# Kernel optimization log

Measured on AMD Instinct MI355X. Metric: run time of the kernel, lower is better.

The kernel has to match this reference:

```python
import jax, jax.numpy as jnp
import numpy as np

B, T, S = 4, 16, 4096
H, KV, D, DIM = 32, 8, 128, 4096
BASE = 10000.0
START = 2048
SCALE = 1.0 / np.sqrt(D)


def _rope(t, cos, sin):
    # t: [B, T, nh, D]; ggml 'normal' rope rotates adjacent pairs (x[2i], x[2i+1])
    b, tt, nh, d = t.shape
    t2 = t.reshape(b, tt, nh, d // 2, 2)
    x0, x1 = t2[..., 0], t2[..., 1]
    c = cos[None, :, None, :]  # [1, T, 1, D/2]
    s = sin[None, :, None, :]
    r = jnp.stack([x0 * c - x1 * s, x0 * s + x1 * c], axis=-1)
    return r.reshape(b, tt, nh, d)


def setup_inputs() -> dict:
    key = jax.random.key(0)
    ks = jax.random.split(key, 8)
    x = jax.random.normal(ks[0], (B, T, DIM), dtype=jnp.float32)
    k_cache = jax.random.normal(ks[1], (B, S, KV, D), dtype=jnp.float32)
    v_cache = jax.random.normal(ks[2], (B, S, KV, D), dtype=jnp.float32)
    wq = jax.random.normal(ks[3], (H * D, DIM), dtype=jnp.float32) * 0.02
    wk = jax.random.normal(ks[4], (KV * D, DIM), dtype=jnp.float32) * 0.02
    wv = jax.random.normal(ks[5], (KV * D, DIM), dtype=jnp.float32) * 0.02
    wo = jax.random.normal(ks[6], (DIM, H * D), dtype=jnp.float32) * 0.02
    input_pos = jnp.arange(T, dtype=jnp.int32) + START  # contiguous decode chunk
    inv_freq = BASE ** (-jnp.arange(0, D, 2, dtype=jnp.float32) / D)  # [D/2]
    ang = input_pos.astype(jnp.float32)[:, None] * inv_freq[None, :]  # [T, D/2]
    freqs_cos = jnp.cos(ang)
    freqs_sin = jnp.sin(ang)
    # causal mask: kv position <= query absolute position, [T, S] bool
    attn_mask = jnp.arange(S, dtype=jnp.int32)[None, :] <= input_pos[:, None]
    return {"x": x, "freqs_cos": freqs_cos, "freqs_sin": freqs_sin,
            "input_pos": input_pos, "attn_mask": attn_mask,
            "k_cache": k_cache, "v_cache": v_cache,
            "wq": wq, "wk": wk, "wv": wv, "wo": wo}


def reference(x, freqs_cos, freqs_sin, input_pos, attn_mask, k_cache, v_cache, wq, wk, wv, wo):
    b, t, _ = x.shape
    q = (x @ wq.T).reshape(b, t, H, D)
    k = (x @ wk.T).reshape(b, t, KV, D)
    v = (x @ wv.T).reshape(b, t, KV, D)
    q = _rope(q, freqs_cos, freqs_sin)
    k = _rope(k, freqs_cos, freqs_sin)
    # KV-cache scatter (index_copy_ along dim 1)
    kc = k_cache.at[:, input_pos].set(k)  # [B, S, KV, D]
    vc = v_cache.at[:, input_pos].set(v)
    g = H // KV
    qh = q.transpose(0, 2, 1, 3).reshape(b, KV, g, t, D)  # [B, KV, g, T, D]
    kf = kc.transpose(0, 2, 1, 3)  # [B, KV, S, D]
    vf = vc.transpose(0, 2, 1, 3)
    scores = jnp.einsum('bkgtd,bksd->bkgts', qh, kf) * SCALE
    scores = jnp.where(attn_mask[None, None, None], scores, jnp.finfo(scores.dtype).min)
    probs = jax.nn.softmax(scores, axis=-1)
    y = jnp.einsum('bkgts,bksd->bkgtd', probs, vf)  # [B, KV, g, T, D]
    y = y.reshape(b, H, t, D).transpose(0, 2, 1, 3).reshape(b, t, H * D)
    return y @ wo.T
```

## Files before the change

kernel.cpp:

```cpp
#include <hip/hip_runtime.h>
#include <hip/hip_bf16.h>


#define SCALE_F 0.08838834764831845f

typedef __attribute__((ext_vector_type(8))) short bf16x8;
typedef __attribute__((ext_vector_type(4))) float f32x4;

__device__ __forceinline__ unsigned short f2b(float f) {
    __hip_bfloat16 h = __float2bfloat16(f);
    return *reinterpret_cast<unsigned short*>(&h);
}

__device__ __forceinline__ bf16x8 pack8(float4 a, float4 b) {
    bf16x8 r;
    r[0] = (short)f2b(a.x); r[1] = (short)f2b(a.y); r[2] = (short)f2b(a.z); r[3] = (short)f2b(a.w);
    r[4] = (short)f2b(b.x); r[5] = (short)f2b(b.y); r[6] = (short)f2b(b.z); r[7] = (short)f2b(b.w);
    return r;
}

__device__ __forceinline__ void gl_lds16(const void* g, void* l) {
    __builtin_amdgcn_global_load_lds(
        (const __attribute__((address_space(1))) void*)g,
        (__attribute__((address_space(3))) void*)l, 16, 0, 0);
}

__global__ __launch_bounds__(256) void xcvt_kernel(
    const float* __restrict__ x, unsigned short* __restrict__ xb)
{
    const int i = (blockIdx.x * 256 + threadIdx.x) * 4;
    float4 v = *(const float4*)(x + i);
    ushort4 o; o.x = f2b(v.x); o.y = f2b(v.y); o.z = f2b(v.z); o.w = f2b(v.w);
    *(ushort4*)(xb + i) = o;
}

__global__ __launch_bounds__(256) void qkv_gemm_kernel(
    const unsigned short* __restrict__ xb,
    const float* __restrict__ wq, const float* __restrict__ wk, const float* __restrict__ wvp,
    float* __restrict__ part)
{
    __shared__ float wlds[2][16][256];
    const int tid = threadIdx.x, lane = tid & 63, wid = tid >> 6;
    const int l15 = lane & 15, lh = lane >> 4;
    const int n0 = blockIdx.x * 32;
    const int kbase = blockIdx.y * 256;

    const float* wptr; int nn;
    if (n0 < 4096)      { wptr = wq;  nn = n0; }
    else if (n0 < 5120) { wptr = wk;  nn = n0 - 4096; }
    else                { wptr = wvp; nn = n0 - 5120; }

    bf16x8 aq[8];
    {
        const unsigned short* ap = xb + (size_t)(16 * wid + l15) * 4096 + kbase + 8 * lh;
        #pragma unroll
        for (int t = 0; t < 8; ++t) aq[t] = *(const bf16x8*)(ap + t * 32);
    }
    asm volatile("" ::: "memory");

    #pragma unroll
    for (int g = 0; g < 2; ++g) {
        #pragma unroll
        for (int i = 0; i < 4; ++i) {
            const int r = wid * 4 + i;
            const float* src = wptr + (size_t)(nn + g * 16 + r) * 4096 + kbase
                             + ((lane ^ (r & 7)) * 4);
            gl_lds16(src, &wlds[g][r][0]);
        }
        asm volatile("" ::: "memory");
    }

    f32x4 acc[2];
    acc[0] = (f32x4){0.f,0.f,0.f,0.f};
    acc[1] = (f32x4){0.f,0.f,0.f,0.f};

    const int key = l15 & 7;
    #pragma unroll
    for (int g = 0; g < 2; ++g) {
        if (g == 0) asm volatile("s_waitcnt vmcnt(4)" ::: "memory");
        else        asm volatile("s_waitcnt vmcnt(0)" ::: "memory");
        __builtin_amdgcn_s_barrier();
        const float* wrow = &wlds[g][l15][0];
        #pragma unroll
        for (int t = 0; t < 8; ++t) {
            const int c0 = (t * 8 + 2 * lh) ^ key;
            const int c1 = (t * 8 + 2 * lh + 1) ^ key;
            float4 w0 = *(const float4*)(wrow + c0 * 4);
            float4 w1 = *(const float4*)(wrow + c1 * 4);
            bf16x8 b = pack8(w0, w1);
            acc[g] = __builtin_amdgcn_mfma_f32_16x16x32_bf16(aq[t], b, acc[g], 0, 0, 0);
        }
    }

    float* pp = part + (size_t)blockIdx.y * 64 * 6144 + n0;
    #pragma unroll
    for (int g = 0; g < 2; ++g)
        #pragma unroll
        for (int r = 0; r < 4; ++r)
            pp[(16 * wid + 4 * lh + r) * 6144 + g * 16 + l15] = acc[g][r];
}

__global__ __launch_bounds__(256) void qkv_reduce_kernel(
    const float* __restrict__ part,
    const float* __restrict__ fcos, const float* __restrict__ fsin,
    unsigned short* __restrict__ q_out, unsigned short* __restrict__ k_new,
    unsigned short* __restrict__ v_new)
{
    const int gid = blockIdx.x * 256 + threadIdx.x;
    const int m = gid / 1536;
    const int n = (gid % 1536) * 4;
    float4 s = {0.f,0.f,0.f,0.f};
    #pragma unroll
    for (int sp = 0; sp < 16; ++sp) {
        float4 v = *(const float4*)(part + (size_t)(sp * 64 + m) * 6144 + n);
        s.x += v.x; s.y += v.y; s.z += v.z; s.w += v.w;
    }
    const int t = m & 15, b = m >> 4;
    ushort4 o;
    if (n < 5120) {
        int d = n & 127;
        float c0 = fcos[t * 64 + (d >> 1)],     s0 = fsin[t * 64 + (d >> 1)];
        float c1 = fcos[t * 64 + (d >> 1) + 1], s1 = fsin[t * 64 + (d >> 1) + 1];
        o.x = f2b(s.x * c0 - s.y * s0);
        o.y = f2b(s.x * s0 + s.y * c0);
        o.z = f2b(s.z * c1 - s.w * s1);
        o.w = f2b(s.z * s1 + s.w * c1);
    } else {
        o.x = f2b(s.x); o.y = f2b(s.y); o.z = f2b(s.z); o.w = f2b(s.w);
    }
    if (n < 4096) {
        int h = n >> 7, d = n & 127;
        int row = (b * 8 + (h >> 2)) * 64 + (h & 3) * 16 + t;
        *(ushort4*)(q_out + row * 128 + d) = o;
    } else if (n < 5120) {
        int idx = n - 4096, kvh = idx >> 7, d = idx & 127;
        *(ushort4*)(k_new + ((b * 8 + kvh) * 16 + t) * 128 + d) = o;
    } else {
        int idx = n - 5120, kvh = idx >> 7, d = idx & 127;
        *(ushort4*)(v_new + ((b * 8 + kvh) * 16 + t) * 128 + d) = o;
    }
}

__global__ __launch_bounds__(256) void attn_kernel(
    const float* __restrict__ k_cache, const float* __restrict__ v_cache,
    const unsigned short* __restrict__ q_glob,
    const unsigned short* __restrict__ k_new, const unsigned short* __restrict__ v_new,
    float* __restrict__ y_part, float* __restrict__ ml)
{
    __shared__ unsigned short smem[32256];
    unsigned short* kv_lds = smem;
    unsigned short* p_lds  = smem + 21504;

    const int bk = blockIdx.x >> 4;
    const int c  = blockIdx.x & 15;
    const int b = bk >> 3, kvh = bk & 7;
    const int tid = threadIdx.x, lane = tid & 63, wid = tid >> 6;
    const int s0 = c * 128;
    const bool last = (c == 15);

    bf16x8 aq[4];
    {
        const unsigned short* qp = q_glob + (bk * 64 + 16 * wid + (lane & 15)) * 128 + 8 * (lane >> 4);
        #pragma unroll
        for (int kk = 0; kk < 4; ++kk) aq[kk] = *(const bf16x8*)(qp + kk * 32);
    }

    const int rr = tid >> 5, ln4 = (tid & 31) * 4;
    {
        const float* kb = k_cache + ((size_t)(b * 4096 + s0) * 8 + kvh) * 128;
        #pragma unroll 4
        for (int it = 0; it < 16; ++it) {
            int srow = it * 8 + rr;
            float4 kf = *(const float4*)(kb + (size_t)srow * 1024 + ln4);
            ushort4 k4; k4.x = f2b(kf.x); k4.y = f2b(kf.y); k4.z = f2b(kf.z); k4.w = f2b(kf.w);
            *(ushort4*)&kv_lds[srow * 136 + ln4] = k4;
        }
        if (last) {
            int row = tid >> 4, c8 = (tid & 15) * 8;
            *(bf16x8*)&kv_lds[(128 + row) * 136 + c8] =
                *(const bf16x8*)(k_new + (bk * 16 + row) * 128 + c8);
        }
    }
    __syncthreads();

    f32x4 sc[9];
    f32x4 zero4 = {0.f,0.f,0.f,0.f};
    #pragma unroll
    for (int st = 0; st < 9; ++st) sc[st] = zero4;
    #pragma unroll
    for (int kk = 0; kk < 4; ++kk) {
        #pragma unroll
        for (int st = 0; st < 9; ++st) {
            if (st == 8 && !last) continue;
            bf16x8 bf = *(bf16x8*)&kv_lds[(st * 16 + (lane & 15)) * 136 + kk * 32 + 8 * (lane >> 4)];
            sc[st] = __builtin_amdgcn_mfma_f32_16x16x32_bf16(aq[kk], bf, sc[st], 0, 0, 0);
        }
    }

    float mrow[4], lrow[4];
    #pragma unroll
    for (int r = 0; r < 4; ++r) {
        int trow = 4 * (lane >> 4) + r;
        float mx = -3.0e38f;
        #pragma unroll
        for (int st = 0; st < 9; ++st) {
            if (st == 8 && !last) continue;
            float s = sc[st][r] * SCALE_F;
            if (st == 8 && (lane & 15) > trow) s = -3.0e38f;
            sc[st][r] = s;
            mx = fmaxf(mx, s);
        }
        mx = fmaxf(mx, __shfl_xor(mx, 1));
        mx = fmaxf(mx, __shfl_xor(mx, 2));
        mx = fmaxf(mx, __shfl_xor(mx, 4));
        mx = fmaxf(mx, __shfl_xor(mx, 8));
        float sum = 0.f;
        #pragma unroll
        for (int st = 0; st < 9; ++st) {
            if (st == 8 && !last) continue;
            float p = __expf(sc[st][r] - mx);
            sc[st][r] = p;
            sum += p;
        }
        sum += __shfl_xor(sum, 1);
        sum += __shfl_xor(sum, 2);
        sum += __shfl_xor(sum, 4);
        sum += __shfl_xor(sum, 8);
        mrow[r] = mx; lrow[r] = sum;
    }

    #pragma unroll
    for (int st = 0; st < 9; ++st) {
        if (st == 8 && !last) continue;
        #pragma unroll
        for (int r = 0; r < 4; ++r)
            p_lds[(16 * wid + 4 * (lane >> 4) + r) * 168 + st * 16 + (lane & 15)] = f2b(sc[st][r]);
    }
    if ((lane & 15) == 0) {
        #pragma unroll
        for (int r = 0; r < 4; ++r) {
            int row = 16 * wid + 4 * (lane >> 4) + r;
            ml[(bk * 16 + c) * 128 + row * 2 + 0] = mrow[r];
            ml[(bk * 16 + c) * 128 + row * 2 + 1] = lrow[r];
        }
    }
    __syncthreads();

    {
        const float* vb = v_cache + ((size_t)(b * 4096 + s0) * 8 + kvh) * 128;
        #pragma unroll 4
        for (int it = 0; it < 16; ++it) {
            int srow = it * 8 + rr;
            float4 vf = *(const float4*)(vb + (size_t)srow * 1024 + ln4);
            kv_lds[(ln4 + 0) * 168 + srow] = f2b(vf.x);
            kv_lds[(ln4 + 1) * 168 + srow] = f2b(vf.y);
            kv_lds[(ln4 + 2) * 168 + srow] = f2b(vf.z);
            kv_lds[(ln4 + 3) * 168 + srow] = f2b(vf.w);
        }
        if (last) {
            int row = tid >> 4, c8 = (tid & 15) * 8;
            bf16x8 vv = *(const bf16x8*)(v_new + (bk * 16 + row) * 128 + c8);
            #pragma unroll
            for (int u = 0; u < 8; ++u)
                kv_lds[(c8 + u) * 168 + 128 + row] = (unsigned short)vv[u];
            int pr = tid >> 2, pc = (tid & 3) * 4;
            #pragma unroll
            for (int u = 0; u < 4; ++u) p_lds[pr * 168 + 144 + pc + u] = 0;
            int vr = tid >> 1, vc = (tid & 1) * 8;
            #pragma unroll
            for (int u = 0; u < 8; ++u) kv_lds[vr * 168 + 144 + vc + u] = 0;
        }
    }
    __syncthreads();

    f32x4 o_[8];
    #pragma unroll
    for (int nt = 0; nt < 8; ++nt) o_[nt] = zero4;
    #pragma unroll
    for (int ks = 0; ks < 5; ++ks) {
        if (ks == 4 && !last) continue;
        bf16x8 a = *(bf16x8*)&p_lds[(16 * wid + (lane & 15)) * 168 + ks * 32 + 8 * (lane >> 4)];
        #pragma unroll
        for (int nt = 0; nt < 8; ++nt) {
            bf16x8 bf = *(bf16x8*)&kv_lds[(nt * 16 + (lane & 15)) * 168 + ks * 32 + 8 * (lane >> 4)];
            o_[nt] = __builtin_amdgcn_mfma_f32_16x16x32_bf16(a, bf, o_[nt], 0, 0, 0);
        }
    }
    float* yp = y_part + (size_t)(bk * 16 + c) * 8192;
    #pragma unroll
    for (int nt = 0; nt < 8; ++nt) {
        #pragma unroll
        for (int r = 0; r < 4; ++r)
            yp[(16 * wid + 4 * (lane >> 4) + r) * 128 + nt * 16 + (lane & 15)] = o_[nt][r];
    }
}

__global__ __launch_bounds__(256) void combine_kernel(
    const float* __restrict__ y_part, const float* __restrict__ ml,
    unsigned short* __restrict__ y_attn)
{
    const int bid = blockIdx.x;
    const int bk = bid >> 3, rg = bid & 7;
    const int b = bk >> 3, kvh = bk & 7;
    const int tid = threadIdx.x;
    const int d = tid & 127, r2 = tid >> 7;
    for (int rr = 0; rr < 8; rr += 2) {
        int row = rg * 8 + rr + r2;
        float mv[16], lv[16], M = -3.0e38f;
        #pragma unroll
        for (int cc = 0; cc < 16; ++cc) {
            mv[cc] = ml[(bk * 16 + cc) * 128 + row * 2 + 0];
            lv[cc] = ml[(bk * 16 + cc) * 128 + row * 2 + 1];
            M = fmaxf(M, mv[cc]);
        }
        float den = 0.f, acc = 0.f;
        #pragma unroll
        for (int cc = 0; cc < 16; ++cc) {
            float co = __expf(mv[cc] - M);
            den += co * lv[cc];
            acc += co * y_part[((size_t)(bk * 16 + cc) * 64 + row) * 128 + d];
        }
        float y = acc / den;
        int gi = row >> 4, t = row & 15;
        y_attn[(b * 16 + t) * 4096 + (kvh * 4 + gi) * 128 + d] = f2b(y);
    }
}

__global__ __launch_bounds__(256) void proj_gemm_kernel(
    const unsigned short* __restrict__ y_attn, const float* __restrict__ wo,
    float* __restrict__ part)
{
    __shared__ float wlds[2][16][256];
    const int tid = threadIdx.x, lane = tid & 63, wid = tid >> 6;
    const int l15 = lane & 15, lh = lane >> 4;
    const int n0 = blockIdx.x * 32;
    const int kbase = blockIdx.y * 256;

    bf16x8 aq[8];
    {
        const unsigned short* ap = y_attn + (size_t)(16 * wid + l15) * 4096 + kbase + 8 * lh;
        #pragma unroll
        for (int t = 0; t < 8; ++t) aq[t] = *(const bf16x8*)(ap + t * 32);
    }
    asm volatile("" ::: "memory");

    #pragma unroll
    for (int g = 0; g < 2; ++g) {
        #pragma unroll
        for (int i = 0; i < 4; ++i) {
            const int r = wid * 4 + i;
            const float* src = wo + (size_t)(n0 + g * 16 + r) * 4096 + kbase
                             + ((lane ^ (r & 7)) * 4);
            gl_lds16(src, &wlds[g][r][0]);
        }
        asm volatile("" ::: "memory");
    }

    f32x4 acc[2];
    acc[0] = (f32x4){0.f,0.f,0.f,0.f};
    acc[1] = (f32x4){0.f,0.f,0.f,0.f};

    const int key = l15 & 7;
    #pragma unroll
    for (int g = 0; g < 2; ++g) {
        if (g == 0) asm volatile("s_waitcnt vmcnt(4)" ::: "memory");
        else        asm volatile("s_waitcnt vmcnt(0)" ::: "memory");
        __builtin_amdgcn_s_barrier();
        const float* wrow = &wlds[g][l15][0];
        #pragma unroll
        for (int t = 0; t < 8; ++t) {
            const int c0 = (t * 8 + 2 * lh) ^ key;
            const int c1 = (t * 8 + 2 * lh + 1) ^ key;
            float4 w0 = *(const float4*)(wrow + c0 * 4);
            float4 w1 = *(const float4*)(wrow + c1 * 4);
            bf16x8 b = pack8(w0, w1);
            acc[g] = __builtin_amdgcn_mfma_f32_16x16x32_bf16(aq[t], b, acc[g], 0, 0, 0);
        }
    }

    float* pp = part + (size_t)blockIdx.y * 64 * 4096 + n0;
    #pragma unroll
    for (int g = 0; g < 2; ++g)
        #pragma unroll
        for (int r = 0; r < 4; ++r)
            pp[(16 * wid + 4 * lh + r) * 4096 + g * 16 + l15] = acc[g][r];
}

__global__ __launch_bounds__(256) void proj_reduce_kernel(
    const float* __restrict__ part, float* __restrict__ out)
{
    const int gid = blockIdx.x * 256 + threadIdx.x;
    const int m = gid >> 10;
    const int n = (gid & 1023) * 4;
    float4 s = {0.f,0.f,0.f,0.f};
    #pragma unroll
    for (int sp = 0; sp < 16; ++sp) {
        float4 v = *(const float4*)(part + (size_t)(sp * 64 + m) * 4096 + n);
        s.x += v.x; s.y += v.y; s.z += v.z; s.w += v.w;
    }
    *(float4*)(out + (size_t)m * 4096 + n) = s;
}

extern "C" void kernel_launch(void* const* d_in, const int* in_sizes, int n_in,
                              void* d_out, int out_size, void* d_ws, size_t ws_size,
                              hipStream_t stream)
{
    const float* x       = (const float*)d_in[0];
    const float* fcos    = (const float*)d_in[1];
    const float* fsin    = (const float*)d_in[2];
    const float* k_cache = (const float*)d_in[5];
    const float* v_cache = (const float*)d_in[6];
    const float* wq      = (const float*)d_in[7];
    const float* wk      = (const float*)d_in[8];
    const float* wv      = (const float*)d_in[9];
    const float* wo      = (const float*)d_in[10];

    char* p = (char*)d_ws;
    unsigned short* q_out  = (unsigned short*)p; p += 4 * 8 * 64 * 128 * 2;
    unsigned short* k_new  = (unsigned short*)p; p += 4 * 8 * 16 * 128 * 2;
    unsigned short* v_new  = (unsigned short*)p; p += 4 * 8 * 16 * 128 * 2;
    unsigned short* y_attn = (unsigned short*)p; p += 64 * 4096 * 2;
    unsigned short* x_bf16 = (unsigned short*)p; p += 64 * 4096 * 2;
    float* mlbuf  = (float*)p; p += 32 * 16 * 64 * 2 * 4;
    float* y_part = (float*)p; p += (size_t)32 * 16 * 64 * 128 * 4;
    float* bigbuf = (float*)p;

    xcvt_kernel<<<256, 256, 0, stream>>>(x, x_bf16);
    qkv_gemm_kernel<<<dim3(192, 16), 256, 0, stream>>>(x_bf16, wq, wk, wv, bigbuf);
    qkv_reduce_kernel<<<384, 256, 0, stream>>>(bigbuf, fcos, fsin, q_out, k_new, v_new);
    attn_kernel<<<512, 256, 0, stream>>>(k_cache, v_cache, q_out, k_new, v_new, y_part, mlbuf);
    combine_kernel<<<256, 256, 0, stream>>>(y_part, mlbuf, y_attn);
    proj_gemm_kernel<<<dim3(128, 16), 256, 0, stream>>>(y_attn, wo, bigbuf);
    proj_reduce_kernel<<<256, 256, 0, stream>>>(bigbuf, (float*)d_out);
}
```

Before: 97.39 us.

## Pipeline GEMM K-loop with 4-stage LDS ring and swizzled bf16 activation layout

Both skinny GEMMs now walk a 512-wide K slice per block in 32-element chunks. Weight and activation tiles are streamed into a 4-buffer LDS ring with async global-to-LDS loads issued two chunks ahead, replacing the old single-shot 256-wide load. The split-K factor drops from 16 to 8, which halves the partial-sum traffic in the reduce kernels but also halves the grid and the parallelism. Activations (x and y_attn) are written in a chunked, XOR-swizzled layout so each chunk is one contiguous copy into LDS, and the per-chunk barriers add sync overhead.

```diff
diff --git a/kernel.cpp b/kernel.cpp
--- a/kernel.cpp
+++ b/kernel.cpp
@@ -25,79 +25,87 @@
         (__attribute__((address_space(3))) void*)l, 16, 0, 0);
 }
 
+
 __global__ __launch_bounds__(256) void xcvt_kernel(
     const float* __restrict__ x, unsigned short* __restrict__ xb)
 {
-    const int i = (blockIdx.x * 256 + threadIdx.x) * 4;
-    float4 v = *(const float4*)(x + i);
-    ushort4 o; o.x = f2b(v.x); o.y = f2b(v.y); o.z = f2b(v.z); o.w = f2b(v.w);
-    *(ushort4*)(xb + i) = o;
-}
+    const int flat = blockIdx.x * 256 + threadIdx.x;
+    const int m = flat >> 9, rem = flat & 511;
+    const int c = rem >> 2, j = rem & 3;
+    const float* src = x + (size_t)m * 4096 + c * 32 + j * 8;
+    float4 a = *(const float4*)src, b = *(const float4*)(src + 4);
+    *(bf16x8*)(xb + c * 2048 + m * 32 + ((j ^ (m & 3)) * 8)) = pack8(a, b);
+}
+
+#define GEMM_BODY(WPTR, NN, LDW, APTR, CG_BASE, NCHUNK, ACC)                                   \
+    const int l15 = lane & 15, lh = lane >> 4;                                                 \
+    const int wr8 = lane >> 3, wc8 = lane & 7;                                                 \
+    const float* wsrc = (WPTR) + (size_t)((NN) + 8 * wid + wr8) * (LDW)                        \
+                      + ((wc8 ^ (wr8 & 7)) * 4);                                               \
+    const unsigned short* asrc = (APTR) + (size_t)(CG_BASE) * 2048 + wid * 512 + lane * 8;     \
+    float* wdst = &wlds[0][0] + wid * 256;                                \
+    unsigned short* adst = &alds[0][0] + wid * 512;                     \
+    _Pragma("unroll")                                                                          \
+    for (int pc = 0; pc < 2; ++pc) {                                                           \
+        gl_lds16(wsrc + (size_t)pc * 32, wdst + (size_t)pc * 1024);                            \
+        gl_lds16(asrc + (size_t)pc * 2048, adst + (size_t)pc * 2048);                          \
+    }                                                                                          \
+    const int key = l15 & 7;                                                                   \
+    const int akey = (l15 & 3);                                                                \
+    for (int c = 0; c < (NCHUNK); ++c) {                                                       \
+        if (c + 2 < (NCHUNK)) {                                                                \
+            const int bq = (c + 2) & 3;                                                        \
+            gl_lds16(wsrc + (size_t)(c + 2) * 32, wdst + (size_t)bq * 1024);                   \
+            gl_lds16(asrc + (size_t)(c + 2) * 2048, adst + (size_t)bq * 2048);                 \
+        }                                                                                      \
+        if (c + 2 < (NCHUNK))      asm volatile("s_waitcnt vmcnt(4)" ::: "memory");            \
+        else if (c + 1 < (NCHUNK)) asm volatile("s_waitcnt vmcnt(2)" ::: "memory");            \
+        else                       asm volatile("s_waitcnt vmcnt(0)" ::: "memory");            \
+        __builtin_amdgcn_s_barrier();                                                          \
+        const int buf = c & 3;                                                                 \
+        const float* wt = &wlds[buf][0];                                                       \
+        const unsigned short* at = &alds[buf][0];                                              \
+        const int arow = 16 * wid + l15;                                                       \
+        bf16x8 a = *(const bf16x8*)(at + arow * 32 + ((lh ^ akey) * 8));                       \
+        const float* w0p = wt + l15 * 32;                                                      \
+        const float* w1p = wt + (16 + l15) * 32;                                               \
+        const int c0 = ((2 * lh) ^ key) * 4, c1 = ((2 * lh + 1) ^ key) * 4;                    \
+        bf16x8 b0 = pack8(*(const float4*)(w0p + c0), *(const float4*)(w0p + c1));             \
+        bf16x8 b1 = pack8(*(const float4*)(w1p + c0), *(const float4*)(w1p + c1));             \
+        ACC[0] = __builtin_amdgcn_mfma_f32_16x16x32_bf16(a, b0, ACC[0], 0, 0, 0);              \
+        ACC[1] = __builtin_amdgcn_mfma_f32_16x16x32_bf16(a, b1, ACC[1], 0, 0, 0);              \
+        __builtin_amdgcn_s_barrier();                                                          \
+    }
 
 __global__ __launch_bounds__(256) void qkv_gemm_kernel(
     const unsigned short* __restrict__ xb,
     const float* __restrict__ wq, const float* __restrict__ wk, const float* __restrict__ wvp,
     float* __restrict__ part)
 {
-    __shared__ float wlds[2][16][256];
+    __shared__ float wlds[4][1024];
+    __shared__ unsigned short alds[4][2048];
     const int tid = threadIdx.x, lane = tid & 63, wid = tid >> 6;
-    const int l15 = lane & 15, lh = lane >> 4;
     const int n0 = blockIdx.x * 32;
-    const int kbase = blockIdx.y * 256;
+    const int split = blockIdx.y;
 
     const float* wptr; int nn;
     if (n0 < 4096)      { wptr = wq;  nn = n0; }
     else if (n0 < 5120) { wptr = wk;  nn = n0 - 4096; }
     else                { wptr = wvp; nn = n0 - 5120; }
 
-    bf16x8 aq[8];
-    {
-        const unsigned short* ap = xb + (size_t)(16 * wid + l15) * 4096 + kbase + 8 * lh;
-        #pragma unroll
-        for (int t = 0; t < 8; ++t) aq[t] = *(const bf16x8*)(ap + t * 32);
-    }
-    asm volatile("" ::: "memory");
-
-    #pragma unroll
-    for (int g = 0; g < 2; ++g) {
-        #pragma unroll
-        for (int i = 0; i < 4; ++i) {
-            const int r = wid * 4 + i;
-            const float* src = wptr + (size_t)(nn + g * 16 + r) * 4096 + kbase
-                             + ((lane ^ (r & 7)) * 4);
-            gl_lds16(src, &wlds[g][r][0]);
-        }
-        asm volatile("" ::: "memory");
-    }
-
     f32x4 acc[2];
     acc[0] = (f32x4){0.f,0.f,0.f,0.f};
     acc[1] = (f32x4){0.f,0.f,0.f,0.f};
 
-    const int key = l15 & 7;
-    #pragma unroll
-    for (int g = 0; g < 2; ++g) {
-        if (g == 0) asm volatile("s_waitcnt vmcnt(4)" ::: "memory");
-        else        asm volatile("s_waitcnt vmcnt(0)" ::: "memory");
-        __builtin_amdgcn_s_barrier();
-        const float* wrow = &wlds[g][l15][0];
-        #pragma unroll
-        for (int t = 0; t < 8; ++t) {
-            const int c0 = (t * 8 + 2 * lh) ^ key;
-            const int c1 = (t * 8 + 2 * lh + 1) ^ key;
-            float4 w0 = *(const float4*)(wrow + c0 * 4);
-            float4 w1 = *(const float4*)(wrow + c1 * 4);
-            bf16x8 b = pack8(w0, w1);
-            acc[g] = __builtin_amdgcn_mfma_f32_16x16x32_bf16(aq[t], b, acc[g], 0, 0, 0);
-        }
-    }
-
-    float* pp = part + (size_t)blockIdx.y * 64 * 6144 + n0;
-    #pragma unroll
-    for (int g = 0; g < 2; ++g)
+    const float* wbase = wptr + split * 512;
+    GEMM_BODY(wbase, nn, 4096, xb, split * 16, 16, acc)
+
+    float* pp = part + (size_t)split * 64 * 6144 + n0;
+    #pragma unroll
+    for (int nh = 0; nh < 2; ++nh)
         #pragma unroll
         for (int r = 0; r < 4; ++r)
-            pp[(16 * wid + 4 * lh + r) * 6144 + g * 16 + l15] = acc[g][r];
+            pp[(16 * wid + 4 * (lane >> 4) + r) * 6144 + nh * 16 + (lane & 15)] = acc[nh][r];
 }
 
 __global__ __launch_bounds__(256) void qkv_reduce_kernel(
@@ -111,7 +119,7 @@
     const int n = (gid % 1536) * 4;
     float4 s = {0.f,0.f,0.f,0.f};
     #pragma unroll
-    for (int sp = 0; sp < 16; ++sp) {
+    for (int sp = 0; sp < 8; ++sp) {
         float4 v = *(const float4*)(part + (size_t)(sp * 64 + m) * 6144 + n);
         s.x += v.x; s.y += v.y; s.z += v.z; s.w += v.w;
     }
@@ -322,7 +330,10 @@
         }
         float y = acc / den;
         int gi = row >> 4, t = row & 15;
-        y_attn[(b * 16 + t) * 4096 + (kvh * 4 + gi) * 128 + d] = f2b(y);
+        int m = b * 16 + t;
+        int n = (kvh * 4 + gi) * 128 + d;
+        int c = n >> 5, j = (n >> 3) & 3, lo = n & 7;
+        y_attn[c * 2048 + m * 32 + ((j ^ (m & 3)) * 8) + lo] = f2b(y);
     }
 }
 
@@ -330,60 +341,25 @@
     const unsigned short* __restrict__ y_attn, const float* __restrict__ wo,
     float* __restrict__ part)
 {
-    __shared__ float wlds[2][16][256];
+    __shared__ float wlds[4][1024];
+    __shared__ unsigned short alds[4][2048];
     const int tid = threadIdx.x, lane = tid & 63, wid = tid >> 6;
-    const int l15 = lane & 15, lh = lane >> 4;
     const int n0 = blockIdx.x * 32;
-    const int kbase = blockIdx.y * 256;
-
-    bf16x8 aq[8];
-    {
-        const unsigned short* ap = y_attn + (size_t)(16 * wid + l15) * 4096 + kbase + 8 * lh;
-        #pragma unroll
-        for (int t = 0; t < 8; ++t) aq[t] = *(const bf16x8*)(ap + t * 32);
-    }
-    asm volatile("" ::: "memory");
-
-    #pragma unroll
-    for (int g = 0; g < 2; ++g) {
-        #pragma unroll
-        for (int i = 0; i < 4; ++i) {
-            const int r = wid * 4 + i;
-            const float* src = wo + (size_t)(n0 + g * 16 + r) * 4096 + kbase
-                             + ((lane ^ (r & 7)) * 4);
-            gl_lds16(src, &wlds[g][r][0]);
-        }
-        asm volatile("" ::: "memory");
-    }
+    const int split = blockIdx.y;
 
     f32x4 acc[2];
     acc[0] = (f32x4){0.f,0.f,0.f,0.f};
     acc[1] = (f32x4){0.f,0.f,0.f,0.f};
 
-    const int key = l15 & 7;
-    #pragma unroll
-    for (int g = 0; g < 2; ++g) {
-        if (g == 0) asm volatile("s_waitcnt vmcnt(4)" ::: "memory");
-        else        asm volatile("s_waitcnt vmcnt(0)" ::: "memory");
-        __builtin_amdgcn_s_barrier();
-        const float* wrow = &wlds[g][l15][0];
-        #pragma unroll
-        for (int t = 0; t < 8; ++t) {
-            const int c0 = (t * 8 + 2 * lh) ^ key;
-            const int c1 = (t * 8 + 2 * lh + 1) ^ key;
-            float4 w0 = *(const float4*)(wrow + c0 * 4);
-            float4 w1 = *(const float4*)(wrow + c1 * 4);
-            bf16x8 b = pack8(w0, w1);
-            acc[g] = __builtin_amdgcn_mfma_f32_16x16x32_bf16(aq[t], b, acc[g], 0, 0, 0);
-        }
-    }
-
-    float* pp = part + (size_t)blockIdx.y * 64 * 4096 + n0;
-    #pragma unroll
-    for (int g = 0; g < 2; ++g)
+    const float* wbase = wo + split * 512;
+    GEMM_BODY(wbase, n0, 4096, y_attn, split * 16, 16, acc)
+
+    float* pp = part + (size_t)split * 64 * 4096 + n0;
+    #pragma unroll
+    for (int nh = 0; nh < 2; ++nh)
         #pragma unroll
         for (int r = 0; r < 4; ++r)
-            pp[(16 * wid + 4 * lh + r) * 4096 + g * 16 + l15] = acc[g][r];
+            pp[(16 * wid + 4 * (lane >> 4) + r) * 4096 + nh * 16 + (lane & 15)] = acc[nh][r];
 }
 
 __global__ __launch_bounds__(256) void proj_reduce_kernel(
@@ -394,7 +370,7 @@
     const int n = (gid & 1023) * 4;
     float4 s = {0.f,0.f,0.f,0.f};
     #pragma unroll
-    for (int sp = 0; sp < 16; ++sp) {
+    for (int sp = 0; sp < 8; ++sp) {
         float4 v = *(const float4*)(part + (size_t)(sp * 64 + m) * 4096 + n);
         s.x += v.x; s.y += v.y; s.z += v.z; s.w += v.w;
     }
@@ -425,11 +401,11 @@
     float* y_part = (float*)p; p += (size_t)32 * 16 * 64 * 128 * 4;
     float* bigbuf = (float*)p;
 
-    xcvt_kernel<<<256, 256, 0, stream>>>(x, x_bf16);
-    qkv_gemm_kernel<<<dim3(192, 16), 256, 0, stream>>>(x_bf16, wq, wk, wv, bigbuf);
+    xcvt_kernel<<<128, 256, 0, stream>>>(x, x_bf16);
+    qkv_gemm_kernel<<<dim3(192, 8), 256, 0, stream>>>(x_bf16, wq, wk, wv, bigbuf);
     qkv_reduce_kernel<<<384, 256, 0, stream>>>(bigbuf, fcos, fsin, q_out, k_new, v_new);
     attn_kernel<<<512, 256, 0, stream>>>(k_cache, v_cache, q_out, k_new, v_new, y_part, mlbuf);
     combine_kernel<<<256, 256, 0, stream>>>(y_part, mlbuf, y_attn);
-    proj_gemm_kernel<<<dim3(128, 16), 256, 0, stream>>>(y_attn, wo, bigbuf);
+    proj_gemm_kernel<<<dim3(128, 8), 256, 0, stream>>>(y_attn, wo, bigbuf);
     proj_reduce_kernel<<<256, 256, 0, stream>>>(bigbuf, (float*)d_out);
 }
```

Measured after the change: 85.65 us. 1.14x faster.
